# Optimization experiments

Hardware: AMD Instinct MI355X
Metric: run time of the kernel (lower is better)

## Reference

```python
import jax, jax.numpy as jnp
import numpy as np

N = 100000
D = 64
H = 4 * D  # 256
E = 1000000


def setup_inputs() -> dict:
    key = jax.random.key(0)
    ks = jax.random.split(key, 9)
    return {
        "loc_feat": jax.random.normal(ks[0], (N, D), dtype=jnp.float32),
        "geo_src": jax.random.randint(ks[1], (E,), 0, N),
        "geo_dst": jax.random.randint(ks[2], (E,), 0, N),
        "trans_src": jax.random.randint(ks[3], (E,), 0, N),
        "trans_dst": jax.random.randint(ks[4], (E,), 0, N),
        "trans_w": jax.random.uniform(ks[5], (E,), dtype=jnp.float32),
        "W1": jax.random.normal(ks[6], (D, H), dtype=jnp.float32) * (1.0 / np.sqrt(D)),
        "b1": jax.random.normal(ks[7], (H,), dtype=jnp.float32) * 0.01,
        "W2": jax.random.normal(ks[8], (H, 1), dtype=jnp.float32) * (1.0 / np.sqrt(H)),
    }


def reference(loc_feat, geo_src, geo_dst, trans_src, trans_dst, trans_w, W1, b1, W2):
    n = loc_feat.shape[0]
    # etype 'geo': copy_u + mean  -> segment mean of src features at dst
    geo_sum = jax.ops.segment_sum(loc_feat[geo_src], geo_dst, num_segments=n)
    cnt = jax.ops.segment_sum(jnp.ones(geo_src.shape[0], loc_feat.dtype), geo_dst, num_segments=n)
    geo = jnp.where(cnt[:, None] > 0, geo_sum / jnp.maximum(cnt, 1.0)[:, None], 0.0)
    # etype 'trans': u_mul_e + sum -> weighted segment sum
    trans = jax.ops.segment_sum(loc_feat[trans_src] * trans_w[:, None], trans_dst, num_segments=n)
    # semantic attention fuse over the two relation views
    z = jnp.stack([geo, trans], axis=1)          # [N, 2, D]
    h = jnp.tanh(jnp.einsum('nkd,dh->nkh', z, W1) + b1)  # [N, 2, H]
    w = jnp.einsum('nkh,ho->nko', h, W2).mean(0)  # [2, 1] (mean over nodes)
    beta = jax.nn.softmax(w, axis=0)              # [2, 1]
    return (beta[None, :, :] * z).sum(1)          # [N, D]
```

## Files before the change

kernel.cpp:

```cpp
#include <hip/hip_runtime.h>
#include <hip/hip_bf16.h>

#define N_NODES 100000
#define DIM 64
#define HID 256
#define E_EDGES 1000000
#define TWO_N (2 * N_NODES)
#define MLP_ROWBLOCKS (TWO_N / 64)

#define TILE 120
#define NBINS 834
#define CAP 1600
#define EPB 4096
#define FILL_BLOCKS 245

typedef short short8 __attribute__((ext_vector_type(8)));
typedef float f32x4 __attribute__((ext_vector_type(4)));
typedef unsigned short us4 __attribute__((ext_vector_type(4)));

__device__ __forceinline__ float tanh_fast(float x) {
    x = fminf(fmaxf(x, -15.0f), 15.0f);
    float e = __expf(2.0f * x);
    return (e - 1.0f) / (e + 1.0f);
}

__device__ __forceinline__ unsigned short f2bf(float x) {
    unsigned u = __float_as_uint(x);
    u = u + 0x7FFFu + ((u >> 16) & 1u);
    return (unsigned short)(u >> 16);
}

__device__ __forceinline__ float bf2f(unsigned short u) {
    return __uint_as_float(((unsigned)u) << 16);
}

__global__ void pack_feat_kernel(const float* __restrict__ feat,
                                 unsigned short* __restrict__ fb) {
    int i = blockIdx.x * 256 + threadIdx.x;
    float4 v = ((const float4*)feat)[i];
    us4 o;
    o[0] = f2bf(v.x); o[1] = f2bf(v.y); o[2] = f2bf(v.z); o[3] = f2bf(v.w);
    ((us4*)fb)[i] = o;
}

__global__ void __launch_bounds__(512) bin_fill_kernel(
        const int* __restrict__ gs, const int* __restrict__ gd,
        const int* __restrict__ ts, const int* __restrict__ td,
        const float* __restrict__ tw,
        int* __restrict__ gcount,
        int* __restrict__ gbin, int2* __restrict__ tbin) {
    __shared__ int   hist[NBINS];
    __shared__ int   adjS[NBINS];
    __shared__ int   curS[NBINS];
    __shared__ int   pS[EPB];
    __shared__ float w2S[EPB];
    __shared__ unsigned short binS[EPB];
    __shared__ int   scanS[512];

    int t = threadIdx.x;
    int blk = blockIdx.x;
    int rel = (blk >= FILL_BLOCKS) ? 1 : 0;
    int e0 = (rel ? blk - FILL_BLOCKS : blk) * EPB;
    const int* dstp = rel ? td : gd;
    const int* srcp = rel ? ts : gs;

    for (int i = t; i < NBINS; i += 512) hist[i] = 0;
    __syncthreads();

    int d_[8], s_[8];
    float w_[8];
    #pragma unroll
    for (int j = 0; j < 2; ++j) {
        int idx = e0 + j * 2048 + 4 * t;
        if (idx + 3 < E_EDGES) {
            int4 dv = *(const int4*)&dstp[idx];
            int4 sv = *(const int4*)&srcp[idx];
            d_[4*j+0] = dv.x; d_[4*j+1] = dv.y; d_[4*j+2] = dv.z; d_[4*j+3] = dv.w;
            s_[4*j+0] = sv.x; s_[4*j+1] = sv.y; s_[4*j+2] = sv.z; s_[4*j+3] = sv.w;
            if (rel) {
                float4 wv = *(const float4*)&tw[idx];
                w_[4*j+0] = wv.x; w_[4*j+1] = wv.y; w_[4*j+2] = wv.z; w_[4*j+3] = wv.w;
            }
        } else {
            #pragma unroll
            for (int i2 = 0; i2 < 4; ++i2) {
                bool ok = (idx + i2 < E_EDGES);
                d_[4*j+i2] = ok ? dstp[idx + i2] : -1;
                s_[4*j+i2] = ok ? srcp[idx + i2] : 0;
                w_[4*j+i2] = (ok && rel) ? tw[idx + i2] : 0.0f;
            }
        }
    }
    #pragma unroll
    for (int i = 0; i < 8; ++i)
        if (d_[i] >= 0) atomicAdd(&hist[d_[i] / TILE], 1);
    __syncthreads();

    int carry = 0;
    for (int cb = 0; cb < NBINS; cb += 512) {
        int i = cb + t;
        int c = (i < NBINS) ? hist[i] : 0;
        __syncthreads();
        scanS[t] = c;
        __syncthreads();
        int v = c;
        #pragma unroll
        for (int off = 1; off < 512; off <<= 1) {
            int add = (t >= off) ? scanS[t - off] : 0;
            __syncthreads();
            v += add;
            scanS[t] = v;
            __syncthreads();
        }
        if (i < NBINS) {
            int lb = v - c + carry;
            curS[i] = lb;
            int gb = (c > 0) ? (i * CAP + atomicAdd(&gcount[rel * NBINS + i], c)) : 0;
            adjS[i] = gb - lb;
        }
        carry += scanS[511];
    }
    __syncthreads();

    #pragma unroll
    for (int i = 0; i < 8; ++i) {
        int d = d_[i];
        if (d < 0) continue;
        int bin = d / TILE;
        int pos = atomicAdd(&curS[bin], 1);
        pS[pos] = s_[i] | ((d - bin * TILE) << 20);
        binS[pos] = (unsigned short)bin;
        if (rel) w2S[pos] = w_[i];
    }
    __syncthreads();

    int nV = min(EPB, E_EDGES - e0);
    if (!rel) {
        for (int i = t; i < nV; i += 512) {
            int b = binS[i];
            int gi = adjS[b] + i;
            if (gi < (b + 1) * CAP)
                gbin[gi] = pS[i];
        }
    } else {
        for (int i = t; i < nV; i += 512) {
            int b = binS[i];
            int gi = adjS[b] + i;
            if (gi < (b + 1) * CAP)
                tbin[gi] = make_int2(pS[i], __float_as_int(w2S[i]));
        }
    }
}

__global__ void __launch_bounds__(256) aggregate_kernel(
        const unsigned short* __restrict__ featb,
        const int* __restrict__ gbin, const int2* __restrict__ tbin,
        const int* __restrict__ gcount,
        unsigned short* __restrict__ zb) {
    __shared__ int   srcS[CAP];
    __shared__ float wS[CAP];
    __shared__ int   histS[TILE];
    __shared__ int   baseS[TILE];
    __shared__ int   curS[TILE];
    __shared__ int   scanS[128];

    int b = blockIdx.x;
    int rel = (b >= NBINS) ? 1 : 0;
    int bin = rel ? b - NBINS : b;
    int node0 = bin * TILE;
    int nNodes = min(TILE, N_NODES - node0);
    int t = threadIdx.x, lane = t & 63, wave = t >> 6;
    int q = lane >> 4, ql = lane & 15;

    int nE = gcount[b];
    if (nE > CAP) nE = CAP;

    for (int i = t; i < TILE; i += 256) histS[i] = 0;
    __syncthreads();

    if (!rel) {
        const int* bp = gbin + (size_t)bin * CAP;
        for (int i = t; i < nE; i += 256) atomicAdd(&histS[bp[i] >> 20], 1);
    } else {
        const int2* bp = tbin + (size_t)bin * CAP;
        for (int i = t; i < nE; i += 256) atomicAdd(&histS[bp[i].x >> 20], 1);
    }
    __syncthreads();

    if (t < 128) scanS[t] = (t < TILE) ? histS[t] : 0;
    __syncthreads();
    #pragma unroll
    for (int off = 1; off < 128; off <<= 1) {
        int add = 0;
        if (t < 128 && t >= off) add = scanS[t - off];
        __syncthreads();
        if (t < 128) scanS[t] += add;
        __syncthreads();
    }
    if (t < TILE) {
        int base = scanS[t] - histS[t];
        baseS[t] = base;
        curS[t] = base;
    }
    __syncthreads();

    if (!rel) {
        const int* bp = gbin + (size_t)bin * CAP;
        for (int i = t; i < nE; i += 256) {
            int p = bp[i];
            int pos = atomicAdd(&curS[p >> 20], 1);
            srcS[pos] = p & 0xFFFFF;
        }
    } else {
        const int2* bp = tbin + (size_t)bin * CAP;
        for (int i = t; i < nE; i += 256) {
            int2 p = bp[i];
            int pos = atomicAdd(&curS[p.x >> 20], 1);
            srcS[pos] = p.x & 0xFFFFF;
            wS[pos] = __int_as_float(p.y);
        }
    }
    __syncthreads();

    for (int nl0 = wave * 4; nl0 < nNodes; nl0 += 16) {
        int nl = nl0 + q;
        bool act = (nl < nNodes);
        int deg = act ? histS[nl] : 0;
        int base = act ? baseS[nl] : 0;
        float a0 = 0.f, a1 = 0.f, a2 = 0.f, a3 = 0.f;
        if (!rel) {
            int k = 0;
            for (; k + 3 < deg; k += 4) {
                int s0 = srcS[base + k], s1 = srcS[base + k + 1];
                int s2 = srcS[base + k + 2], s3 = srcS[base + k + 3];
                us4 r0 = *(const us4*)&featb[(size_t)s0 * DIM + ql * 4];
                us4 r1 = *(const us4*)&featb[(size_t)s1 * DIM + ql * 4];
                us4 r2 = *(const us4*)&featb[(size_t)s2 * DIM + ql * 4];
                us4 r3 = *(const us4*)&featb[(size_t)s3 * DIM + ql * 4];
                a0 += (bf2f(r0[0]) + bf2f(r1[0])) + (bf2f(r2[0]) + bf2f(r3[0]));
                a1 += (bf2f(r0[1]) + bf2f(r1[1])) + (bf2f(r2[1]) + bf2f(r3[1]));
                a2 += (bf2f(r0[2]) + bf2f(r1[2])) + (bf2f(r2[2]) + bf2f(r3[2]));
                a3 += (bf2f(r0[3]) + bf2f(r1[3])) + (bf2f(r2[3]) + bf2f(r3[3]));
            }
            for (; k < deg; ++k) {
                int s = srcS[base + k];
                us4 r = *(const us4*)&featb[(size_t)s * DIM + ql * 4];
                a0 += bf2f(r[0]); a1 += bf2f(r[1]);
                a2 += bf2f(r[2]); a3 += bf2f(r[3]);
            }
        } else {
            int k = 0;
            for (; k + 3 < deg; k += 4) {
                int s0 = srcS[base + k], s1 = srcS[base + k + 1];
                int s2 = srcS[base + k + 2], s3 = srcS[base + k + 3];
                float w0 = wS[base + k], w1 = wS[base + k + 1];
                float w2 = wS[base + k + 2], w3 = wS[base + k + 3];
                us4 r0 = *(const us4*)&featb[(size_t)s0 * DIM + ql * 4];
                us4 r1 = *(const us4*)&featb[(size_t)s1 * DIM + ql * 4];
                us4 r2 = *(const us4*)&featb[(size_t)s2 * DIM + ql * 4];
                us4 r3 = *(const us4*)&featb[(size_t)s3 * DIM + ql * 4];
                a0 += (bf2f(r0[0]) * w0 + bf2f(r1[0]) * w1) + (bf2f(r2[0]) * w2 + bf2f(r3[0]) * w3);
                a1 += (bf2f(r0[1]) * w0 + bf2f(r1[1]) * w1) + (bf2f(r2[1]) * w2 + bf2f(r3[1]) * w3);
                a2 += (bf2f(r0[2]) * w0 + bf2f(r1[2]) * w1) + (bf2f(r2[2]) * w2 + bf2f(r3[2]) * w3);
                a3 += (bf2f(r0[3]) * w0 + bf2f(r1[3]) * w1) + (bf2f(r2[3]) * w2 + bf2f(r3[3]) * w3);
            }
            for (; k < deg; ++k) {
                int s = srcS[base + k];
                float w = wS[base + k];
                us4 r = *(const us4*)&featb[(size_t)s * DIM + ql * 4];
                a0 += bf2f(r[0]) * w; a1 += bf2f(r[1]) * w;
                a2 += bf2f(r[2]) * w; a3 += bf2f(r[3]) * w;
            }
        }
        if (act) {
            float sc = rel ? 1.0f : 1.0f / fmaxf((float)deg, 1.0f);
            us4 o;
            o[0] = f2bf(a0 * sc); o[1] = f2bf(a1 * sc);
            o[2] = f2bf(a2 * sc); o[3] = f2bf(a3 * sc);
            size_t row = (size_t)(rel ? N_NODES + node0 + nl : node0 + nl);
            *(us4*)&zb[row * DIM + ql * 4] = o;
        }
    }
}

__global__ void pack_w1_kernel(const float* __restrict__ W1, unsigned short* __restrict__ W1p) {
    int i = blockIdx.x * 256 + threadIdx.x;
    int j = i & 7;
    int r = i >> 3;
    int nidx = r & 15; r >>= 4;
    int q = r & 3; r >>= 2;
    int khalf = r & 1;
    int n = r >> 1;
    int k = 32 * khalf + 8 * q + j;
    int c = 16 * n + nidx;
    W1p[i] = f2bf(W1[k * HID + c]);
}

__global__ void __launch_bounds__(256) mlp_mfma_kernel(
        const unsigned short* __restrict__ zb,
        const unsigned short* __restrict__ W1p,
        const float* __restrict__ bias1, const float* __restrict__ W2,
        float* __restrict__ partials) {
    __shared__ float wred[4][2];
    int t = threadIdx.x, lane = t & 63, wave = t >> 6;
    int m = lane & 15, q = lane >> 4;
    int base = blockIdx.x * 64 + wave * 16;
    int R = base + m;

    const unsigned short* rowp = zb + (size_t)R * DIM;
    short8 a0 = *(const short8*)(rowp + q * 8);
    short8 a1 = *(const short8*)(rowp + 32 + q * 8);

    float c0 = 0.0f, c1 = 0.0f;
    const short8* W1v = (const short8*)W1p;

    #pragma unroll 4
    for (int n = 0; n < 16; ++n) {
        short8 b0 = W1v[(n * 2 + 0) * 64 + lane];
        short8 bK = W1v[(n * 2 + 1) * 64 + lane];
        f32x4 acc = {0.0f, 0.0f, 0.0f, 0.0f};
        acc = __builtin_amdgcn_mfma_f32_16x16x32_bf16(a0, b0, acc, 0, 0, 0);
        acc = __builtin_amdgcn_mfma_f32_16x16x32_bf16(a1, bK, acc, 0, 0, 0);
        int col = 16 * n + m;
        float bj = bias1[col];
        float w2 = W2[col];
        #pragma unroll
        for (int reg = 0; reg < 4; ++reg) {
            int Rr = base + q * 4 + reg;
            float h = tanh_fast(acc[reg] + bj);
            float contrib = h * w2;
            if (Rr < N_NODES) c0 += contrib; else c1 += contrib;
        }
    }

    #pragma unroll
    for (int off = 32; off > 0; off >>= 1) {
        c0 += __shfl_down(c0, off);
        c1 += __shfl_down(c1, off);
    }
    if (lane == 0) { wred[wave][0] = c0; wred[wave][1] = c1; }
    __syncthreads();
    if (t == 0) {
        partials[blockIdx.x * 2 + 0] = wred[0][0] + wred[1][0] + wred[2][0] + wred[3][0];
        partials[blockIdx.x * 2 + 1] = wred[0][1] + wred[1][1] + wred[2][1] + wred[3][1];
    }
}

__global__ void beta_kernel(const float* __restrict__ partials, float* __restrict__ beta) {
    __shared__ float wred[4][2];
    int t = threadIdx.x;
    float c0 = 0.0f, c1 = 0.0f;
    for (int i = t; i < MLP_ROWBLOCKS; i += 256) {
        c0 += partials[i * 2 + 0];
        c1 += partials[i * 2 + 1];
    }
    #pragma unroll
    for (int off = 32; off > 0; off >>= 1) {
        c0 += __shfl_down(c0, off);
        c1 += __shfl_down(c1, off);
    }
    int lane = t & 63, wv = t >> 6;
    if (lane == 0) { wred[wv][0] = c0; wred[wv][1] = c1; }
    __syncthreads();
    if (t == 0) {
        float s0 = (wred[0][0] + wred[1][0] + wred[2][0] + wred[3][0]) / (float)N_NODES;
        float s1 = (wred[0][1] + wred[1][1] + wred[2][1] + wred[3][1]) / (float)N_NODES;
        float m = fmaxf(s0, s1);
        float e0 = __expf(s0 - m), e1 = __expf(s1 - m);
        float inv = 1.0f / (e0 + e1);
        beta[0] = e0 * inv;
        beta[1] = e1 * inv;
    }
}

__global__ void combine_kernel(const unsigned short* __restrict__ zb,
                               const float* __restrict__ beta,
                               float* __restrict__ out) {
    int gid = blockIdx.x * 256 + threadIdx.x;
    float b0 = beta[0];
    float b1 = beta[1];
    uint4 g = *(const uint4*)&zb[(size_t)gid * 8];
    uint4 tr = *(const uint4*)&zb[(size_t)N_NODES * DIM + (size_t)gid * 8];
    float4 o0, o1;
    o0.x = b0 * __uint_as_float(g.x << 16) + b1 * __uint_as_float(tr.x << 16);
    o0.y = b0 * __uint_as_float(g.x & 0xFFFF0000u) + b1 * __uint_as_float(tr.x & 0xFFFF0000u);
    o0.z = b0 * __uint_as_float(g.y << 16) + b1 * __uint_as_float(tr.y << 16);
    o0.w = b0 * __uint_as_float(g.y & 0xFFFF0000u) + b1 * __uint_as_float(tr.y & 0xFFFF0000u);
    o1.x = b0 * __uint_as_float(g.z << 16) + b1 * __uint_as_float(tr.z << 16);
    o1.y = b0 * __uint_as_float(g.z & 0xFFFF0000u) + b1 * __uint_as_float(tr.z & 0xFFFF0000u);
    o1.z = b0 * __uint_as_float(g.w << 16) + b1 * __uint_as_float(tr.w << 16);
    o1.w = b0 * __uint_as_float(g.w & 0xFFFF0000u) + b1 * __uint_as_float(tr.w & 0xFFFF0000u);
    *(float4*)&out[(size_t)gid * 8] = o0;
    *(float4*)&out[(size_t)gid * 8 + 4] = o1;
}

extern "C" void kernel_launch(void* const* d_in, const int* in_sizes, int n_in,
                              void* d_out, int out_size, void* d_ws, size_t ws_size,
                              hipStream_t stream) {
    const float* loc_feat = (const float*)d_in[0];
    const int* geo_src    = (const int*)d_in[1];
    const int* geo_dst    = (const int*)d_in[2];
    const int* trans_src  = (const int*)d_in[3];
    const int* trans_dst  = (const int*)d_in[4];
    const float* trans_w  = (const float*)d_in[5];
    const float* W1       = (const float*)d_in[6];
    const float* b1       = (const float*)d_in[7];
    const float* W2       = (const float*)d_in[8];
    float* out = (float*)d_out;

    int*   gcount   = (int*)d_ws;
    int*   gbin     = gcount + 2 * NBINS;
    int2*  tbin     = (int2*)(gbin + (size_t)NBINS * CAP);
    float* partials = (float*)(tbin + (size_t)NBINS * CAP);
    float* beta     = partials + 2 * MLP_ROWBLOCKS;
    unsigned short* W1p   = (unsigned short*)(beta + 2);
    unsigned short* featb = W1p + 16384;
    unsigned short* zb    = featb + (size_t)N_NODES * DIM;

    hipMemsetAsync(gcount, 0, 2 * NBINS * sizeof(int), stream);

    pack_feat_kernel<<<(N_NODES * DIM / 4) / 256, 256, 0, stream>>>(loc_feat, featb);
    pack_w1_kernel<<<64, 256, 0, stream>>>(W1, W1p);
    bin_fill_kernel<<<2 * FILL_BLOCKS, 512, 0, stream>>>(geo_src, geo_dst, trans_src,
                                                         trans_dst, trans_w,
                                                         gcount, gbin, tbin);
    aggregate_kernel<<<2 * NBINS, 256, 0, stream>>>(featb, gbin, tbin, gcount, zb);
    mlp_mfma_kernel<<<MLP_ROWBLOCKS, 256, 0, stream>>>(zb, W1p, b1, W2, partials);
    beta_kernel<<<1, 256, 0, stream>>>(partials, beta);
    combine_kernel<<<(N_NODES * DIM / 8) / 256, 256, 0, stream>>>(zb, beta, out);
}
```

Baseline: 234.1 us.

## Halve bin tile size, use wave-shuffle scans, and 8-wide bf16 gathers

Shrinks node tiles from 120 to 60 (doubling bin count and halving per-bin capacity) so more aggregate blocks run with smaller shared-memory footprints. The block-wide shared-memory scans in the binning and aggregation kernels are replaced with wave-level shuffle scans, which need fewer barriers. The gather loop now has each lane load 8 bf16 values (16 bytes) instead of 4, so one wave covers 8 nodes per iteration. The trade-offs are more global bin counters and atomics in the fill kernel, and a higher risk of overflowing the smaller per-bin capacity, which would silently drop edges.

```diff
diff --git a/kernel.cpp b/kernel.cpp
--- a/kernel.cpp
+++ b/kernel.cpp
@@ -8,15 +8,16 @@
 #define TWO_N (2 * N_NODES)
 #define MLP_ROWBLOCKS (TWO_N / 64)
 
-#define TILE 120
-#define NBINS 834
-#define CAP 1600
+#define TILE 60
+#define NBINS 1667
+#define CAP 800
 #define EPB 4096
 #define FILL_BLOCKS 245
 
 typedef short short8 __attribute__((ext_vector_type(8)));
 typedef float f32x4 __attribute__((ext_vector_type(4)));
 typedef unsigned short us4 __attribute__((ext_vector_type(4)));
+typedef unsigned short us8 __attribute__((ext_vector_type(8)));
 
 __device__ __forceinline__ float tanh_fast(float x) {
     x = fminf(fmaxf(x, -15.0f), 15.0f);
@@ -55,9 +56,11 @@
     __shared__ int   pS[EPB];
     __shared__ float w2S[EPB];
     __shared__ unsigned short binS[EPB];
-    __shared__ int   scanS[512];
+    __shared__ int   wsumS[8];
+    __shared__ int   wpreS[8];
 
     int t = threadIdx.x;
+    int lane = t & 63, wv = t >> 6;
     int blk = blockIdx.x;
     int rel = (blk >= FILL_BLOCKS) ? 1 : 0;
     int e0 = (rel ? blk - FILL_BLOCKS : blk) * EPB;
@@ -78,8 +81,8 @@
             d_[4*j+0] = dv.x; d_[4*j+1] = dv.y; d_[4*j+2] = dv.z; d_[4*j+3] = dv.w;
             s_[4*j+0] = sv.x; s_[4*j+1] = sv.y; s_[4*j+2] = sv.z; s_[4*j+3] = sv.w;
             if (rel) {
-                float4 wv = *(const float4*)&tw[idx];
-                w_[4*j+0] = wv.x; w_[4*j+1] = wv.y; w_[4*j+2] = wv.z; w_[4*j+3] = wv.w;
+                float4 wvv = *(const float4*)&tw[idx];
+                w_[4*j+0] = wvv.x; w_[4*j+1] = wvv.y; w_[4*j+2] = wvv.z; w_[4*j+3] = wvv.w;
             }
         } else {
             #pragma unroll
@@ -100,25 +103,29 @@
     for (int cb = 0; cb < NBINS; cb += 512) {
         int i = cb + t;
         int c = (i < NBINS) ? hist[i] : 0;
-        __syncthreads();
-        scanS[t] = c;
-        __syncthreads();
         int v = c;
         #pragma unroll
-        for (int off = 1; off < 512; off <<= 1) {
-            int add = (t >= off) ? scanS[t - off] : 0;
-            __syncthreads();
-            v += add;
-            scanS[t] = v;
-            __syncthreads();
-        }
+        for (int off = 1; off < 64; off <<= 1) {
+            int u = __shfl_up(v, off);
+            if (lane >= off) v += u;
+        }
+        if (lane == 63) wsumS[wv] = v;
+        __syncthreads();
+        if (t == 0) {
+            int s = 0;
+            #pragma unroll
+            for (int w = 0; w < 8; ++w) { s += wsumS[w]; wpreS[w] = s; }
+        }
+        __syncthreads();
+        int woff = (wv == 0) ? 0 : wpreS[wv - 1];
         if (i < NBINS) {
-            int lb = v - c + carry;
+            int lb = carry + woff + v - c;
             curS[i] = lb;
             int gb = (c > 0) ? (i * CAP + atomicAdd(&gcount[rel * NBINS + i], c)) : 0;
             adjS[i] = gb - lb;
         }
-        carry += scanS[511];
+        carry += wpreS[7];
+        __syncthreads();
     }
     __syncthreads();
 
@@ -162,7 +169,6 @@
     __shared__ int   histS[TILE];
     __shared__ int   baseS[TILE];
     __shared__ int   curS[TILE];
-    __shared__ int   scanS[128];
 
     int b = blockIdx.x;
     int rel = (b >= NBINS) ? 1 : 0;
@@ -170,7 +176,8 @@
     int node0 = bin * TILE;
     int nNodes = min(TILE, N_NODES - node0);
     int t = threadIdx.x, lane = t & 63, wave = t >> 6;
-    int q = lane >> 4, ql = lane & 15;
+    int oct = lane >> 3;
+    int co = (lane & 7) * 8;
 
     int nE = gcount[b];
     if (nE > CAP) nE = CAP;
@@ -187,20 +194,19 @@
     }
     __syncthreads();
 
-    if (t < 128) scanS[t] = (t < TILE) ? histS[t] : 0;
-    __syncthreads();
-    #pragma unroll
-    for (int off = 1; off < 128; off <<= 1) {
-        int add = 0;
-        if (t < 128 && t >= off) add = scanS[t - off];
-        __syncthreads();
-        if (t < 128) scanS[t] += add;
-        __syncthreads();
-    }
-    if (t < TILE) {
-        int base = scanS[t] - histS[t];
-        baseS[t] = base;
-        curS[t] = base;
+    if (t < 64) {
+        int c = (t < TILE) ? histS[t] : 0;
+        int v = c;
+        #pragma unroll
+        for (int off = 1; off < 64; off <<= 1) {
+            int u = __shfl_up(v, off);
+            if (t >= off) v += u;
+        }
+        if (t < TILE) {
+            int b0 = v - c;
+            baseS[t] = b0;
+            curS[t] = b0;
+        }
     }
     __syncthreads();
 
@@ -222,63 +228,62 @@
     }
     __syncthreads();
 
-    for (int nl0 = wave * 4; nl0 < nNodes; nl0 += 16) {
-        int nl = nl0 + q;
+    for (int nl0 = wave * 8; nl0 < nNodes; nl0 += 32) {
+        int nl = nl0 + oct;
         bool act = (nl < nNodes);
         int deg = act ? histS[nl] : 0;
         int base = act ? baseS[nl] : 0;
-        float a0 = 0.f, a1 = 0.f, a2 = 0.f, a3 = 0.f;
+        float a[8] = {0.f, 0.f, 0.f, 0.f, 0.f, 0.f, 0.f, 0.f};
         if (!rel) {
             int k = 0;
             for (; k + 3 < deg; k += 4) {
-                int s0 = srcS[base + k], s1 = srcS[base + k + 1];
+                int s0 = srcS[base + k],     s1 = srcS[base + k + 1];
                 int s2 = srcS[base + k + 2], s3 = srcS[base + k + 3];
-                us4 r0 = *(const us4*)&featb[(size_t)s0 * DIM + ql * 4];
-                us4 r1 = *(const us4*)&featb[(size_t)s1 * DIM + ql * 4];
-                us4 r2 = *(const us4*)&featb[(size_t)s2 * DIM + ql * 4];
-                us4 r3 = *(const us4*)&featb[(size_t)s3 * DIM + ql * 4];
-                a0 += (bf2f(r0[0]) + bf2f(r1[0])) + (bf2f(r2[0]) + bf2f(r3[0]));
-                a1 += (bf2f(r0[1]) + bf2f(r1[1])) + (bf2f(r2[1]) + bf2f(r3[1]));
-                a2 += (bf2f(r0[2]) + bf2f(r1[2])) + (bf2f(r2[2]) + bf2f(r3[2]));
-                a3 += (bf2f(r0[3]) + bf2f(r1[3])) + (bf2f(r2[3]) + bf2f(r3[3]));
+                us8 r0 = *(const us8*)&featb[(size_t)s0 * DIM + co];
+                us8 r1 = *(const us8*)&featb[(size_t)s1 * DIM + co];
+                us8 r2 = *(const us8*)&featb[(size_t)s2 * DIM + co];
+                us8 r3 = *(const us8*)&featb[(size_t)s3 * DIM + co];
+                #pragma unroll
+                for (int j = 0; j < 8; ++j)
+                    a[j] += (bf2f(r0[j]) + bf2f(r1[j])) + (bf2f(r2[j]) + bf2f(r3[j]));
             }
             for (; k < deg; ++k) {
                 int s = srcS[base + k];
-                us4 r = *(const us4*)&featb[(size_t)s * DIM + ql * 4];
-                a0 += bf2f(r[0]); a1 += bf2f(r[1]);
-                a2 += bf2f(r[2]); a3 += bf2f(r[3]);
+                us8 r = *(const us8*)&featb[(size_t)s * DIM + co];
+                #pragma unroll
+                for (int j = 0; j < 8; ++j) a[j] += bf2f(r[j]);
             }
         } else {
             int k = 0;
             for (; k + 3 < deg; k += 4) {
-                int s0 = srcS[base + k], s1 = srcS[base + k + 1];
+                int s0 = srcS[base + k],     s1 = srcS[base + k + 1];
                 int s2 = srcS[base + k + 2], s3 = srcS[base + k + 3];
-                float w0 = wS[base + k], w1 = wS[base + k + 1];
+                float w0 = wS[base + k],     w1 = wS[base + k + 1];
                 float w2 = wS[base + k + 2], w3 = wS[base + k + 3];
-                us4 r0 = *(const us4*)&featb[(size_t)s0 * DIM + ql * 4];
-                us4 r1 = *(const us4*)&featb[(size_t)s1 * DIM + ql * 4];
-                us4 r2 = *(const us4*)&featb[(size_t)s2 * DIM + ql * 4];
-                us4 r3 = *(const us4*)&featb[(size_t)s3 * DIM + ql * 4];
-                a0 += (bf2f(r0[0]) * w0 + bf2f(r1[0]) * w1) + (bf2f(r2[0]) * w2 + bf2f(r3[0]) * w3);
-                a1 += (bf2f(r0[1]) * w0 + bf2f(r1[1]) * w1) + (bf2f(r2[1]) * w2 + bf2f(r3[1]) * w3);
-                a2 += (bf2f(r0[2]) * w0 + bf2f(r1[2]) * w1) + (bf2f(r2[2]) * w2 + bf2f(r3[2]) * w3);
-                a3 += (bf2f(r0[3]) * w0 + bf2f(r1[3]) * w1) + (bf2f(r2[3]) * w2 + bf2f(r3[3]) * w3);
+                us8 r0 = *(const us8*)&featb[(size_t)s0 * DIM + co];
+                us8 r1 = *(const us8*)&featb[(size_t)s1 * DIM + co];
+                us8 r2 = *(const us8*)&featb[(size_t)s2 * DIM + co];
+                us8 r3 = *(const us8*)&featb[(size_t)s3 * DIM + co];
+                #pragma unroll
+                for (int j = 0; j < 8; ++j)
+                    a[j] += (bf2f(r0[j]) * w0 + bf2f(r1[j]) * w1)
+                          + (bf2f(r2[j]) * w2 + bf2f(r3[j]) * w3);
             }
             for (; k < deg; ++k) {
                 int s = srcS[base + k];
                 float w = wS[base + k];
-                us4 r = *(const us4*)&featb[(size_t)s * DIM + ql * 4];
-                a0 += bf2f(r[0]) * w; a1 += bf2f(r[1]) * w;
-                a2 += bf2f(r[2]) * w; a3 += bf2f(r[3]) * w;
+                us8 r = *(const us8*)&featb[(size_t)s * DIM + co];
+                #pragma unroll
+                for (int j = 0; j < 8; ++j) a[j] += bf2f(r[j]) * w;
             }
         }
         if (act) {
             float sc = rel ? 1.0f : 1.0f / fmaxf((float)deg, 1.0f);
-            us4 o;
-            o[0] = f2bf(a0 * sc); o[1] = f2bf(a1 * sc);
-            o[2] = f2bf(a2 * sc); o[3] = f2bf(a3 * sc);
+            us8 o;
+            #pragma unroll
+            for (int j = 0; j < 8; ++j) o[j] = f2bf(a[j] * sc);
             size_t row = (size_t)(rel ? N_NODES + node0 + nl : node0 + nl);
-            *(us4*)&zb[row * DIM + ql * 4] = o;
+            *(us8*)&zb[row * DIM + co] = o;
         }
     }
 }
```

Result: no change. 236.8 us (+1.2%).
